# Optimization experiments

Measured on AMD Instinct MI355X. Metric: run time of the kernel, lower is better.

Reference implementation:

```python
import jax, jax.numpy as jnp
import numpy as np

DIMS = 2048
Q_HEADS = 32
K_HEADS = 8
HEAD_DIM = DIMS // Q_HEADS  # 64
KV_DIM = K_HEADS * HEAD_DIM  # 512
B, S, IN_DIM = 2, 2048, 2048


def setup_inputs() -> dict:
    key = jax.random.key(0)
    ks = jax.random.split(key, 11)
    sc_in = 1.0 / np.sqrt(IN_DIM)
    sc_out = 1.0 / np.sqrt(DIMS)
    return {
        "q": jax.random.normal(ks[0], (B, S, IN_DIM), jnp.float32),
        "k": jax.random.normal(ks[1], (B, S, IN_DIM), jnp.float32),
        "v": jax.random.normal(ks[2], (B, S, IN_DIM), jnp.float32),
        "Wq": jax.random.normal(ks[3], (IN_DIM, DIMS), jnp.float32) * sc_in,
        "bq": jnp.zeros((DIMS,), jnp.float32),
        "Wk": jax.random.normal(ks[4], (IN_DIM, KV_DIM), jnp.float32) * sc_in,
        "bk": jnp.zeros((KV_DIM,), jnp.float32),
        "Wv": jax.random.normal(ks[5], (IN_DIM, KV_DIM), jnp.float32) * sc_in,
        "bv": jnp.zeros((KV_DIM,), jnp.float32),
        "Wo": jax.random.normal(ks[6], (DIMS, IN_DIM), jnp.float32) * sc_out,
        "bo": jnp.zeros((IN_DIM,), jnp.float32),
    }


def reference(q, k, v, Wq, bq, Wk, bk, Wv, bv, Wo, bo):
    rep = Q_HEADS // K_HEADS
    # projections
    qx = (q @ Wq + bq).reshape(B, S, Q_HEADS, HEAD_DIM)
    kx = (k @ Wk + bk).reshape(B, S, K_HEADS, HEAD_DIM)
    vx = (v @ Wv + bv).reshape(B, S, K_HEADS, HEAD_DIM)
    # repeat kv heads to match q heads (matches kx.repeat(rep, axis=-2))
    kx = jnp.repeat(kx, rep, axis=-2)
    vx = jnpp_repeat(vx, rep) if False else jnp.repeat(vx, rep, axis=-2)
    # [B, H, S, D]
    qx = jnp.einsum('bshd->bhsd', qx)
    kx = jnp.einsum('bshd->bhsd', kx)
    vx = jnp.einsum('bshd->bhsd', vx)
    scores = jnp.einsum('bhqd,bhkd->bhqk', qx, kx) / jnp.sqrt(
        jnp.asarray(HEAD_DIM, qx.dtype))
    scores = jax.nn.softmax(scores, axis=-1)
    out = jnp.einsum('bhqk,bhkd->bhqd', scores, vx)
    out = jnp.einsum('bhsd->bshd', out).reshape(B, S, DIMS)
    return out @ Wo + bo
```

## Files before the change

### kernel.cpp

```cpp
#include <hip/hip_runtime.h>
#include <cstdint>
#include <cstddef>

typedef _Float16 half8   __attribute__((ext_vector_type(8)));
typedef _Float16 half4_t __attribute__((ext_vector_type(4)));
typedef __fp16   fp16x2  __attribute__((ext_vector_type(2)));
typedef float    f32x4   __attribute__((ext_vector_type(4)));

typedef __attribute__((address_space(1))) const void GV;
typedef __attribute__((address_space(3))) void LV;

__device__ __forceinline__ void gl_lds16(const _Float16* g, _Float16* l) {
    __builtin_amdgcn_global_load_lds((GV*)g, (LV*)l, 16, 0, 0);
}

#define BB    2
#define SS    2048
#define INDIM 2048
#define DIMS_ 2048
#define QH    32
#define KH_   8
#define HD    64
#define KVD   512
#define RWS   4096

#define QSCALE (0.125f * 1.44269504088896340736f)

__global__ void cast_f16_3(const float* __restrict__ a, const float* __restrict__ b,
                           const float* __restrict__ c,
                           _Float16* __restrict__ oa, _Float16* __restrict__ ob,
                           _Float16* __restrict__ oc) {
    const float* in  = (blockIdx.y == 0) ? a : (blockIdx.y == 1) ? b : c;
    _Float16*    out = (blockIdx.y == 0) ? oa : (blockIdx.y == 1) ? ob : oc;
    int i = (blockIdx.x * 256 + threadIdx.x) * 8;
    const float4* p = (const float4*)(in + i);
    float4 x = p[0], y = p[1];
    half8 h;
    h[0]=(_Float16)x.x; h[1]=(_Float16)x.y; h[2]=(_Float16)x.z; h[3]=(_Float16)x.w;
    h[4]=(_Float16)y.x; h[5]=(_Float16)y.y; h[6]=(_Float16)y.z; h[7]=(_Float16)y.w;
    *(half8*)(out + i) = h;
}

__global__ void transpose_cast2(const float* __restrict__ in0, _Float16* __restrict__ out0,
                                const float* __restrict__ in1, _Float16* __restrict__ out1,
                                int R, int C) {
    const float* in  = blockIdx.z ? in1 : in0;
    _Float16*    out = blockIdx.z ? out1 : out0;
    __shared__ float t[32][33];
    int r0 = blockIdx.y * 32, c0 = blockIdx.x * 32;
    int tx = threadIdx.x, ty = threadIdx.y;
    for (int i = ty; i < 32; i += 8)
        t[i][tx] = in[(size_t)(r0 + i) * C + c0 + tx];
    __syncthreads();
    for (int i = ty; i < 32; i += 8)
        out[(size_t)(c0 + i) * R + r0 + tx] = (_Float16)t[tx][i];
}

__global__ void transpose_v(const _Float16* __restrict__ vx, _Float16* __restrict__ vt) {
    int bk = blockIdx.z; int bb = bk >> 3, kh = bk & 7;
    int s0 = blockIdx.x * 32, d0 = blockIdx.y * 32;
    __shared__ _Float16 t[32][33];
    int tx = threadIdx.x, ty = threadIdx.y;
    for (int i = ty; i < 32; i += 8)
        t[i][tx] = vx[(size_t)(bb * SS + s0 + i) * KVD + kh * HD + d0 + tx];
    __syncthreads();
    for (int i = ty; i < 32; i += 8)
        vt[((size_t)(bb * KH_ + kh) * HD + d0 + i) * SS + s0 + tx] = t[tx][i];
}

template<bool OUTF32>
__global__ __launch_bounds__(256) void gemm_f16(
    const _Float16* A0, const _Float16* B0, const float* bias0, _Float16* Ch0,
    const _Float16* A1, const _Float16* B1, const float* bias1, _Float16* Ch1,
    float* Cf, float scale, int M, int N, int K)
{
    const _Float16* A  = A0;  const _Float16* Bt = B0;
    const float*    bias = bias0;  _Float16* Ch = Ch0;
    if (blockIdx.z) { A = A1; Bt = B1; bias = bias1; Ch = Ch1; }

    const int bn = blockIdx.x, bm = blockIdx.y;
    const int tid = threadIdx.x;
    const int wave = tid >> 6, lane = tid & 63, quad = lane >> 4, l15 = lane & 15;
    const int wm = wave & 1, wn = wave >> 1;

    __shared__ __align__(16) _Float16 As[128 * 32];
    __shared__ __align__(16) _Float16 Bs[128 * 32];

    f32x4 acc[4][4] = {};

    const int kiters = K >> 5;
    for (int kt = 0; kt < kiters; ++kt) {
        __syncthreads();
        const _Float16* Ag = A  + (size_t)(bm * 128) * K + kt * 32;
        const _Float16* Bg = Bt + (size_t)(bn * 128) * K + kt * 32;
#pragma unroll
        for (int i = 0; i < 2; ++i) {
            int f = i * 256 + tid;
            gl_lds16(Ag + (size_t)(f >> 2) * K + (f & 3) * 8,
                     As + (size_t)(i * 256 + (tid & 192)) * 8);
            gl_lds16(Bg + (size_t)(f >> 2) * K + (f & 3) * 8,
                     Bs + (size_t)(i * 256 + (tid & 192)) * 8);
        }
        __syncthreads();

        half8 af[4], bf[4];
#pragma unroll
        for (int i = 0; i < 4; ++i)
            af[i] = *(const half8*)(As + (wm * 64 + i * 16 + l15) * 32 + quad * 8);
#pragma unroll
        for (int j = 0; j < 4; ++j)
            bf[j] = *(const half8*)(Bs + (wn * 64 + j * 16 + l15) * 32 + quad * 8);
#pragma unroll
        for (int i = 0; i < 4; ++i)
#pragma unroll
            for (int j = 0; j < 4; ++j)
                acc[i][j] = __builtin_amdgcn_mfma_f32_16x16x32_f16(af[i], bf[j], acc[i][j], 0, 0, 0);
    }

    const int row0 = bm * 128 + wm * 64;
    const int col0 = bn * 128 + wn * 64;
#pragma unroll
    for (int j = 0; j < 4; ++j) {
        int col = col0 + j * 16 + l15;
        float bv = bias[col];
#pragma unroll
        for (int i = 0; i < 4; ++i) {
#pragma unroll
            for (int r = 0; r < 4; ++r) {
                int row = row0 + i * 16 + quad * 4 + r;
                float v = (acc[i][j][r] + bv) * scale;
                if (OUTF32) Cf[(size_t)row * N + col] = v;
                else        Ch[(size_t)row * N + col] = (_Float16)v;
            }
        }
    }
}

__global__ __launch_bounds__(256) void attn_fused(
    const _Float16* __restrict__ qx, const _Float16* __restrict__ kx,
    const _Float16* __restrict__ vt, _Float16* __restrict__ o16)
{
    const int qt = blockIdx.x;
    const int bh = blockIdx.y;
    const int bb = bh >> 5, h = bh & 31, kh = h >> 2;
    const int tid = threadIdx.x;
    const int w = tid >> 6, lane = tid & 63, quad = lane >> 4, l15 = lane & 15;

    __shared__ __align__(16) _Float16 Ks[64 * 64];
    __shared__ __align__(16) _Float16 Vs[64 * 64];
    __shared__ __align__(16) _Float16 Ps[4][32 * 72];

    const size_t qrow0 = (size_t)bb * SS + (size_t)qt * 128 + w * 32;
    half8 qf[2][2];
#pragma unroll
    for (int nb = 0; nb < 2; ++nb)
#pragma unroll
        for (int kk = 0; kk < 2; ++kk)
            qf[nb][kk] = *(const half8*)(qx + (qrow0 + nb * 16 + l15) * DIMS_
                                            + h * HD + kk * 32 + quad * 8);

    half8 vone;
#pragma unroll
    for (int i = 0; i < 8; ++i) vone[i] = (_Float16)1.0f;

    f32x4 ob[2][4] = {};
    f32x4 lacc[2] = {};

    const _Float16* kbase = kx + (size_t)bb * SS * KVD + kh * HD;
    const _Float16* vbase = vt + (size_t)(bb * KH_ + kh) * HD * SS;
    _Float16* Pw = &Ps[w][0];

    const int srowlo = lane >> 3;
    const int scol   = ((lane & 7) ^ srowlo) * 8;

    for (int kt = 0; kt < SS / 64; ++kt) {
        __syncthreads();
#pragma unroll
        for (int i = 0; i < 2; ++i) {
            int row = w * 16 + i * 8 + srowlo;
            gl_lds16(kbase + (size_t)(kt * 64 + row) * KVD + scol,
                     Ks + (w * 16 + i * 8) * 64);
            gl_lds16(vbase + (size_t)row * SS + kt * 64 + scol,
                     Vs + (w * 16 + i * 8) * 64);
        }
        __syncthreads();

        f32x4 st[4][2] = {};
#pragma unroll
        for (int kk = 0; kk < 2; ++kk) {
            half8 ka[4];
#pragma unroll
            for (int mk = 0; mk < 4; ++mk)
                ka[mk] = *(const half8*)(Ks + (mk * 16 + l15) * 64
                                            + (((kk * 4 + quad) ^ (l15 & 7)) * 8));
#pragma unroll
            for (int mk = 0; mk < 4; ++mk)
#pragma unroll
                for (int nb = 0; nb < 2; ++nb)
                    st[mk][nb] = __builtin_amdgcn_mfma_f32_16x16x32_f16(
                        ka[mk], qf[nb][kk], st[mk][nb], 0, 0, 0);
        }

#pragma unroll
        for (int mk = 0; mk < 4; ++mk)
#pragma unroll
            for (int nb = 0; nb < 2; ++nb) {
                float p0 = __builtin_amdgcn_exp2f(st[mk][nb][0]);
                float p1 = __builtin_amdgcn_exp2f(st[mk][nb][1]);
                float p2 = __builtin_amdgcn_exp2f(st[mk][nb][2]);
                float p3 = __builtin_amdgcn_exp2f(st[mk][nb][3]);
                fp16x2 lo = __builtin_amdgcn_cvt_pkrtz(p0, p1);
                fp16x2 hi = __builtin_amdgcn_cvt_pkrtz(p2, p3);
                half4_t hp;
                hp[0] = (_Float16)lo[0]; hp[1] = (_Float16)lo[1];
                hp[2] = (_Float16)hi[0]; hp[3] = (_Float16)hi[1];
                *(half4_t*)(Pw + (nb * 16 + l15) * 72 + mk * 16 + quad * 4) = hp;
            }

#pragma unroll
        for (int kk = 0; kk < 2; ++kk) {
            half8 pa[2], vb[4];
#pragma unroll
            for (int mb = 0; mb < 2; ++mb)
                pa[mb] = *(const half8*)(Pw + (mb * 16 + l15) * 72 + kk * 32 + quad * 8);
#pragma unroll
            for (int nd = 0; nd < 4; ++nd)
                vb[nd] = *(const half8*)(Vs + (nd * 16 + l15) * 64
                                            + (((kk * 4 + quad) ^ (l15 & 7)) * 8));
#pragma unroll
            for (int mb = 0; mb < 2; ++mb) {
#pragma unroll
                for (int nd = 0; nd < 4; ++nd)
                    ob[mb][nd] = __builtin_amdgcn_mfma_f32_16x16x32_f16(
                        pa[mb], vb[nd], ob[mb][nd], 0, 0, 0);
                lacc[mb] = __builtin_amdgcn_mfma_f32_16x16x32_f16(
                    pa[mb], vone, lacc[mb], 0, 0, 0);
            }
        }
    }

#pragma unroll
    for (int mb = 0; mb < 2; ++mb)
#pragma unroll
        for (int r = 0; r < 4; ++r) {
            float rl = __builtin_amdgcn_rcpf(lacc[mb][r]);
            size_t row = qrow0 + mb * 16 + quad * 4 + r;
#pragma unroll
            for (int nd = 0; nd < 4; ++nd)
                o16[row * DIMS_ + h * HD + nd * 16 + l15] =
                    (_Float16)(ob[mb][nd][r] * rl);
        }
}

extern "C" void kernel_launch(void* const* d_in, const int* in_sizes, int n_in,
                              void* d_out, int out_size, void* d_ws, size_t ws_size,
                              hipStream_t stream) {
    const float* q  = (const float*)d_in[0];
    const float* k  = (const float*)d_in[1];
    const float* v  = (const float*)d_in[2];
    const float* Wq = (const float*)d_in[3];
    const float* bq = (const float*)d_in[4];
    const float* Wk = (const float*)d_in[5];
    const float* bk = (const float*)d_in[6];
    const float* Wv = (const float*)d_in[7];
    const float* bv = (const float*)d_in[8];
    const float* Wo = (const float*)d_in[9];
    const float* bo = (const float*)d_in[10];

    char* ws = (char*)d_ws;
    _Float16* q16  = (_Float16*)ws;  ws += (size_t)RWS * INDIM * 2;
    _Float16* k16  = (_Float16*)ws;  ws += (size_t)RWS * INDIM * 2;
    _Float16* v16  = (_Float16*)ws;  ws += (size_t)RWS * INDIM * 2;
    _Float16* qx16 = (_Float16*)ws;  ws += (size_t)RWS * DIMS_ * 2;
    _Float16* kx16 = (_Float16*)ws;  ws += (size_t)RWS * KVD * 2;
    _Float16* vx16 = (_Float16*)ws;  ws += (size_t)RWS * KVD * 2;
    _Float16* o16  = (_Float16*)ws;  ws += (size_t)RWS * DIMS_ * 2;
    _Float16* WqT  = (_Float16*)ws;  ws += (size_t)DIMS_ * INDIM * 2;
    _Float16* WkT  = (_Float16*)ws;  ws += (size_t)KVD * INDIM * 2;
    _Float16* WvT  = (_Float16*)ws;  ws += (size_t)KVD * INDIM * 2;
    _Float16* WoT  = (_Float16*)ws;  ws += (size_t)INDIM * DIMS_ * 2;
    _Float16* vtg  = (_Float16*)ws;  ws += (size_t)BB * KH_ * HD * SS * 2;

    const int nAct = RWS * INDIM;
    cast_f16_3<<<dim3(nAct / (256 * 8), 3), 256, 0, stream>>>(q, k, v, q16, k16, v16);

    transpose_cast2<<<dim3(DIMS_ / 32, INDIM / 32, 2), dim3(32, 8), 0, stream>>>(
        Wq, WqT, Wo, WoT, INDIM, DIMS_);
    transpose_cast2<<<dim3(KVD / 32, INDIM / 32, 2), dim3(32, 8), 0, stream>>>(
        Wk, WkT, Wv, WvT, INDIM, KVD);

    gemm_f16<false><<<dim3(DIMS_ / 128, RWS / 128, 1), 256, 0, stream>>>(
        q16, WqT, bq, qx16, nullptr, nullptr, nullptr, nullptr,
        nullptr, QSCALE, RWS, DIMS_, INDIM);
    gemm_f16<false><<<dim3(KVD / 128, RWS / 128, 2), 256, 0, stream>>>(
        k16, WkT, bk, kx16, v16, WvT, bv, vx16,
        nullptr, 1.0f, RWS, KVD, INDIM);

    transpose_v<<<dim3(SS / 32, HD / 32, BB * KH_), dim3(32, 8), 0, stream>>>(vx16, vtg);

    attn_fused<<<dim3(SS / 128, BB * QH), 256, 0, stream>>>(qx16, kx16, vtg, o16);

    gemm_f16<true><<<dim3(INDIM / 128, RWS / 128, 1), 256, 0, stream>>>(
        o16, WoT, bo, nullptr, nullptr, nullptr, nullptr, nullptr,
        (float*)d_out, 1.0f, RWS, DIMS_, INDIM);
}
```

Measured before the change: 449.0 us.

## Merge QKV projections into one launch, fuse V transpose, enlarge attention query tile

The Q, K and V projection GEMMs now run as one 768-block launch. The V projection epilogue writes its output directly in transposed per-head layout, which removes the separate transpose_v kernel and the vx intermediate buffer. The attention kernel now processes 256 query rows per block (64 per wave) instead of 128, and gets a launch_bounds occupancy hint. This doubles K/V tile reuse per LDS load, at the cost of more accumulator registers and a larger P buffer in LDS, and it halves the attention grid size.

```diff
diff --git a/kernel.cpp b/kernel.cpp
--- a/kernel.cpp
+++ b/kernel.cpp
@@ -56,29 +56,27 @@
         out[(size_t)(c0 + i) * R + r0 + tx] = (_Float16)t[tx][i];
 }
 
-__global__ void transpose_v(const _Float16* __restrict__ vx, _Float16* __restrict__ vt) {
-    int bk = blockIdx.z; int bb = bk >> 3, kh = bk & 7;
-    int s0 = blockIdx.x * 32, d0 = blockIdx.y * 32;
-    __shared__ _Float16 t[32][33];
-    int tx = threadIdx.x, ty = threadIdx.y;
-    for (int i = ty; i < 32; i += 8)
-        t[i][tx] = vx[(size_t)(bb * SS + s0 + i) * KVD + kh * HD + d0 + tx];
-    __syncthreads();
-    for (int i = ty; i < 32; i += 8)
-        vt[((size_t)(bb * KH_ + kh) * HD + d0 + i) * SS + s0 + tx] = t[tx][i];
-}
-
-template<bool OUTF32>
-__global__ __launch_bounds__(256) void gemm_f16(
-    const _Float16* A0, const _Float16* B0, const float* bias0, _Float16* Ch0,
-    const _Float16* A1, const _Float16* B1, const float* bias1, _Float16* Ch1,
-    float* Cf, float scale, int M, int N, int K)
+__global__ __launch_bounds__(256) void gemm_qkv(
+    const _Float16* __restrict__ q16, const _Float16* __restrict__ k16,
+    const _Float16* __restrict__ v16,
+    const _Float16* __restrict__ WqT, const _Float16* __restrict__ WkT,
+    const _Float16* __restrict__ WvT,
+    const float* __restrict__ bq, const float* __restrict__ bk,
+    const float* __restrict__ bv,
+    _Float16* __restrict__ qx, _Float16* __restrict__ kx,
+    _Float16* __restrict__ vtg)
 {
-    const _Float16* A  = A0;  const _Float16* Bt = B0;
-    const float*    bias = bias0;  _Float16* Ch = Ch0;
-    if (blockIdx.z) { A = A1; Bt = B1; bias = bias1; Ch = Ch1; }
-
-    const int bn = blockIdx.x, bm = blockIdx.y;
+    const int bid = blockIdx.x;
+    const _Float16* A; const _Float16* Bt; const float* bias;
+    int bn, bm, N, mode; float scale;
+    if (bid < 512)      { mode = 0; A = q16; Bt = WqT; bias = bq; N = 2048;
+                          bn = bid & 15; bm = bid >> 4; scale = QSCALE; }
+    else if (bid < 640) { int t = bid - 512; mode = 1; A = k16; Bt = WkT; bias = bk;
+                          N = 512; bn = t & 3; bm = t >> 2; scale = 1.0f; }
+    else                { int t = bid - 640; mode = 2; A = v16; Bt = WvT; bias = bv;
+                          N = 512; bn = t & 3; bm = t >> 2; scale = 1.0f; }
+    const int K = 2048;
+
     const int tid = threadIdx.x;
     const int wave = tid >> 6, lane = tid & 63, quad = lane >> 4, l15 = lane & 15;
     const int wm = wave & 1, wn = wave >> 1;
@@ -88,8 +86,7 @@
 
     f32x4 acc[4][4] = {};
 
-    const int kiters = K >> 5;
-    for (int kt = 0; kt < kiters; ++kt) {
+    for (int kt = 0; kt < K / 32; ++kt) {
         __syncthreads();
         const _Float16* Ag = A  + (size_t)(bm * 128) * K + kt * 32;
         const _Float16* Bg = Bt + (size_t)(bn * 128) * K + kt * 32;
@@ -119,24 +116,99 @@
 
     const int row0 = bm * 128 + wm * 64;
     const int col0 = bn * 128 + wn * 64;
+    if (mode < 2) {
+        _Float16* out = mode ? kx : qx;
+#pragma unroll
+        for (int j = 0; j < 4; ++j) {
+            int col = col0 + j * 16 + l15;
+            float bv_ = bias[col];
+#pragma unroll
+            for (int i = 0; i < 4; ++i)
+#pragma unroll
+                for (int r = 0; r < 4; ++r) {
+                    int row = row0 + i * 16 + quad * 4 + r;
+                    out[(size_t)row * N + col] = (_Float16)((acc[i][j][r] + bv_) * scale);
+                }
+        }
+    } else {
+#pragma unroll
+        for (int j = 0; j < 4; ++j) {
+            int c = col0 + j * 16 + l15;
+            int kh = c >> 6, d = c & 63;
+            float bv_ = bias[c];
+#pragma unroll
+            for (int i = 0; i < 4; ++i) {
+                int row = row0 + i * 16 + quad * 4;
+                int bb2 = row >> 11, s = row & 2047;
+                half4_t hp;
+#pragma unroll
+                for (int r = 0; r < 4; ++r) hp[r] = (_Float16)(acc[i][j][r] + bv_);
+                *(half4_t*)(vtg + ((size_t)(bb2 * KH_ + kh) * HD + d) * SS + s) = hp;
+            }
+        }
+    }
+}
+
+__global__ __launch_bounds__(256) void gemm_oproj(
+    const _Float16* __restrict__ A, const _Float16* __restrict__ Bt,
+    const float* __restrict__ bias, float* __restrict__ Cf)
+{
+    const int N = 2048, K = 2048;
+    const int bn = blockIdx.x, bm = blockIdx.y;
+    const int tid = threadIdx.x;
+    const int wave = tid >> 6, lane = tid & 63, quad = lane >> 4, l15 = lane & 15;
+    const int wm = wave & 1, wn = wave >> 1;
+
+    __shared__ __align__(16) _Float16 As[128 * 32];
+    __shared__ __align__(16) _Float16 Bs[128 * 32];
+
+    f32x4 acc[4][4] = {};
+
+    for (int kt = 0; kt < K / 32; ++kt) {
+        __syncthreads();
+        const _Float16* Ag = A  + (size_t)(bm * 128) * K + kt * 32;
+        const _Float16* Bg = Bt + (size_t)(bn * 128) * K + kt * 32;
+#pragma unroll
+        for (int i = 0; i < 2; ++i) {
+            int f = i * 256 + tid;
+            gl_lds16(Ag + (size_t)(f >> 2) * K + (f & 3) * 8,
+                     As + (size_t)(i * 256 + (tid & 192)) * 8);
+            gl_lds16(Bg + (size_t)(f >> 2) * K + (f & 3) * 8,
+                     Bs + (size_t)(i * 256 + (tid & 192)) * 8);
+        }
+        __syncthreads();
+
+        half8 af[4], bf[4];
+#pragma unroll
+        for (int i = 0; i < 4; ++i)
+            af[i] = *(const half8*)(As + (wm * 64 + i * 16 + l15) * 32 + quad * 8);
+#pragma unroll
+        for (int j = 0; j < 4; ++j)
+            bf[j] = *(const half8*)(Bs + (wn * 64 + j * 16 + l15) * 32 + quad * 8);
+#pragma unroll
+        for (int i = 0; i < 4; ++i)
+#pragma unroll
+            for (int j = 0; j < 4; ++j)
+                acc[i][j] = __builtin_amdgcn_mfma_f32_16x16x32_f16(af[i], bf[j], acc[i][j], 0, 0, 0);
+    }
+
+    const int row0 = bm * 128 + wm * 64;
+    const int col0 = bn * 128 + wn * 64;
 #pragma unroll
     for (int j = 0; j < 4; ++j) {
         int col = col0 + j * 16 + l15;
-        float bv = bias[col];
-#pragma unroll
-        for (int i = 0; i < 4; ++i) {
+        float bv_ = bias[col];
+#pragma unroll
+        for (int i = 0; i < 4; ++i)
 #pragma unroll
             for (int r = 0; r < 4; ++r) {
                 int row = row0 + i * 16 + quad * 4 + r;
-                float v = (acc[i][j][r] + bv) * scale;
-                if (OUTF32) Cf[(size_t)row * N + col] = v;
-                else        Ch[(size_t)row * N + col] = (_Float16)v;
-            }
-        }
-    }
-}
-
-__global__ __launch_bounds__(256) void attn_fused(
+                Cf[(size_t)row * N + col] = acc[i][j][r] + bv_;
+            }
+    }
+}
+
+__global__ __launch_bounds__(256, 2) void attn_fused(
     const _Float16* __restrict__ qx, const _Float16* __restrict__ kx,
     const _Float16* __restrict__ vt, _Float16* __restrict__ o16)
 {
@@ -148,12 +220,12 @@
 
     __shared__ __align__(16) _Float16 Ks[64 * 64];
     __shared__ __align__(16) _Float16 Vs[64 * 64];
-    __shared__ __align__(16) _Float16 Ps[4][32 * 72];
-
-    const size_t qrow0 = (size_t)bb * SS + (size_t)qt * 128 + w * 32;
-    half8 qf[2][2];
-#pragma unroll
-    for (int nb = 0; nb < 2; ++nb)
+    __shared__ __align__(16) _Float16 Ps[4][64 * 72];
+
+    const size_t qrow0 = (size_t)bb * SS + (size_t)qt * 256 + w * 64;
+    half8 qf[4][2];
+#pragma unroll
+    for (int nb = 0; nb < 4; ++nb)
 #pragma unroll
         for (int kk = 0; kk < 2; ++kk)
             qf[nb][kk] = *(const half8*)(qx + (qrow0 + nb * 16 + l15) * DIMS_
@@ -163,8 +235,8 @@
 #pragma unroll
     for (int i = 0; i < 8; ++i) vone[i] = (_Float16)1.0f;
 
-    f32x4 ob[2][4] = {};
-    f32x4 lacc[2] = {};
+    f32x4 ob[4][4] = {};
+    f32x4 lacc[4] = {};
 
     const _Float16* kbase = kx + (size_t)bb * SS * KVD + kh * HD;
     const _Float16* vbase = vt + (size_t)(bb * KH_ + kh) * HD * SS;
@@ -185,30 +257,24 @@
         }
         __syncthreads();
 
-        f32x4 st[4][2] = {};
-#pragma unroll
-        for (int kk = 0; kk < 2; ++kk) {
-            half8 ka[4];
-#pragma unroll
-            for (int mk = 0; mk < 4; ++mk)
-                ka[mk] = *(const half8*)(Ks + (mk * 16 + l15) * 64
-                                            + (((kk * 4 + quad) ^ (l15 & 7)) * 8));
-#pragma unroll
-            for (int mk = 0; mk < 4; ++mk)
-#pragma unroll
-                for (int nb = 0; nb < 2; ++nb)
-                    st[mk][nb] = __builtin_amdgcn_mfma_f32_16x16x32_f16(
-                        ka[mk], qf[nb][kk], st[mk][nb], 0, 0, 0);
-        }
-
-#pragma unroll
-        for (int mk = 0; mk < 4; ++mk)
-#pragma unroll
-            for (int nb = 0; nb < 2; ++nb) {
-                float p0 = __builtin_amdgcn_exp2f(st[mk][nb][0]);
-                float p1 = __builtin_amdgcn_exp2f(st[mk][nb][1]);
-                float p2 = __builtin_amdgcn_exp2f(st[mk][nb][2]);
-                float p3 = __builtin_amdgcn_exp2f(st[mk][nb][3]);
+#pragma unroll
+        for (int mk = 0; mk < 4; ++mk) {
+            f32x4 st4[4] = {};
+#pragma unroll
+            for (int kk = 0; kk < 2; ++kk) {
+                half8 ka = *(const half8*)(Ks + (mk * 16 + l15) * 64
+                                              + (((kk * 4 + quad) ^ (l15 & 7)) * 8));
+#pragma unroll
+                for (int nb = 0; nb < 4; ++nb)
+                    st4[nb] = __builtin_amdgcn_mfma_f32_16x16x32_f16(
+                        ka, qf[nb][kk], st4[nb], 0, 0, 0);
+            }
+#pragma unroll
+            for (int nb = 0; nb < 4; ++nb) {
+                float p0 = __builtin_amdgcn_exp2f(st4[nb][0]);
+                float p1 = __builtin_amdgcn_exp2f(st4[nb][1]);
+                float p2 = __builtin_amdgcn_exp2f(st4[nb][2]);
+                float p3 = __builtin_amdgcn_exp2f(st4[nb][3]);
                 fp16x2 lo = __builtin_amdgcn_cvt_pkrtz(p0, p1);
                 fp16x2 hi = __builtin_amdgcn_cvt_pkrtz(p2, p3);
                 half4_t hp;
@@ -216,19 +282,20 @@
                 hp[2] = (_Float16)hi[0]; hp[3] = (_Float16)hi[1];
                 *(half4_t*)(Pw + (nb * 16 + l15) * 72 + mk * 16 + quad * 4) = hp;
             }
+        }
 
 #pragma unroll
         for (int kk = 0; kk < 2; ++kk) {
-            half8 pa[2], vb[4];
-#pragma unroll
-            for (int mb = 0; mb < 2; ++mb)
+            half8 pa[4], vb[4];
+#pragma unroll
+            for (int mb = 0; mb < 4; ++mb)
                 pa[mb] = *(const half8*)(Pw + (mb * 16 + l15) * 72 + kk * 32 + quad * 8);
 #pragma unroll
             for (int nd = 0; nd < 4; ++nd)
                 vb[nd] = *(const half8*)(Vs + (nd * 16 + l15) * 64
                                             + (((kk * 4 + quad) ^ (l15 & 7)) * 8));
 #pragma unroll
-            for (int mb = 0; mb < 2; ++mb) {
+            for (int mb = 0; mb < 4; ++mb) {
 #pragma unroll
                 for (int nd = 0; nd < 4; ++nd)
                     ob[mb][nd] = __builtin_amdgcn_mfma_f32_16x16x32_f16(
@@ -240,7 +307,7 @@
     }
 
 #pragma unroll
-    for (int mb = 0; mb < 2; ++mb)
+    for (int mb = 0; mb < 4; ++mb)
 #pragma unroll
         for (int r = 0; r < 4; ++r) {
             float rl = __builtin_amdgcn_rcpf(lacc[mb][r]);
@@ -273,7 +340,6 @@
     _Float16* v16  = (_Float16*)ws;  ws += (size_t)RWS * INDIM * 2;
     _Float16* qx16 = (_Float16*)ws;  ws += (size_t)RWS * DIMS_ * 2;
     _Float16* kx16 = (_Float16*)ws;  ws += (size_t)RWS * KVD * 2;
-    _Float16* vx16 = (_Float16*)ws;  ws += (size_t)RWS * KVD * 2;
     _Float16* o16  = (_Float16*)ws;  ws += (size_t)RWS * DIMS_ * 2;
     _Float16* WqT  = (_Float16*)ws;  ws += (size_t)DIMS_ * INDIM * 2;
     _Float16* WkT  = (_Float16*)ws;  ws += (size_t)KVD * INDIM * 2;
@@ -289,18 +355,11 @@
     transpose_cast2<<<dim3(KVD / 32, INDIM / 32, 2), dim3(32, 8), 0, stream>>>(
         Wk, WkT, Wv, WvT, INDIM, KVD);
 
-    gemm_f16<false><<<dim3(DIMS_ / 128, RWS / 128, 1), 256, 0, stream>>>(
-        q16, WqT, bq, qx16, nullptr, nullptr, nullptr, nullptr,
-        nullptr, QSCALE, RWS, DIMS_, INDIM);
-    gemm_f16<false><<<dim3(KVD / 128, RWS / 128, 2), 256, 0, stream>>>(
-        k16, WkT, bk, kx16, v16, WvT, bv, vx16,
-        nullptr, 1.0f, RWS, KVD, INDIM);
-
-    transpose_v<<<dim3(SS / 32, HD / 32, BB * KH_), dim3(32, 8), 0, stream>>>(vx16, vtg);
-
-    attn_fused<<<dim3(SS / 128, BB * QH), 256, 0, stream>>>(qx16, kx16, vtg, o16);
-
-    gemm_f16<true><<<dim3(INDIM / 128, RWS / 128, 1), 256, 0, stream>>>(
-        o16, WoT, bo, nullptr, nullptr, nullptr, nullptr, nullptr,
-        (float*)d_out, 1.0f, RWS, DIMS_, INDIM);
-}
+    gemm_qkv<<<768, 256, 0, stream>>>(q16, k16, v16, WqT, WkT, WvT,
+                                      bq, bk, bv, qx16, kx16, vtg);
+
+    attn_fused<<<dim3(SS / 256, BB * QH), 256, 0, stream>>>(qx16, kx16, vtg, o16);
+
+    gemm_oproj<<<dim3(INDIM / 128, RWS / 128), 256, 0, stream>>>(
+        o16, WoT, bo, (float*)d_out);
+}
```

New measurement: 389.0 us. 13.4% less time.
